# Kernel optimization log

Measured on AMD Instinct MI355X. Metric: run time of the kernel, lower is better.

Reference implementation:

```python
import jax, jax.numpy as jnp
import numpy as np
import math

B, S, HID, H = 1, 2048, 1024, 16
D = HID // H  # head_dim = 64


def setup_inputs() -> dict:
    key = jax.random.key(0)
    ks = jax.random.split(key, 12)
    s = 0.02
    x = jax.random.normal(ks[0], (B, S, HID), jnp.float32)
    Wq = jax.random.normal(ks[1], (HID, HID), jnp.float32) * s
    bq = jnp.zeros((HID,), jnp.float32)
    Wk = jax.random.normal(ks[2], (HID, HID), jnp.float32) * s
    bk = jnp.zeros((HID,), jnp.float32)
    Wv = jax.random.normal(ks[3], (HID, HID), jnp.float32) * s
    bv = jnp.zeros((HID,), jnp.float32)
    Wo = jax.random.normal(ks[4], (HID, HID), jnp.float32) * s
    bo = jnp.zeros((HID,), jnp.float32)
    # nn.Parameter(torch.ones(3,3)) at init; small noise so the bias is non-degenerate
    cmw = jnp.ones((3, 3), jnp.float32) + 0.1 * jax.random.normal(ks[5], (3, 3), jnp.float32)
    # full causal [B,S,S] mask so the mask.shape[1]==seq_len branch is taken
    mask = jnp.tril(jnp.ones((B, S, S), jnp.int32))
    modality_info = jax.random.randint(ks[6], (B, S), 0, 3, dtype=jnp.int64)
    return dict(x=x, Wq=Wq, bq=bq, Wk=Wk, bk=bk, Wv=Wv, bv=bv, Wo=Wo, bo=bo,
                cmw=cmw, mask=mask, modality_info=modality_info)


def reference(x, Wq, bq, Wk, bk, Wv, bv, Wo, bo, cmw, mask, modality_info):
    b, s, _ = x.shape
    # QKV projections (torch Linear: y = x @ W.T + b), split into heads [B,H,S,D]
    q = (x @ Wq.T + bq).reshape(b, s, H, D).transpose(0, 2, 1, 3)
    k = (x @ Wk.T + bk).reshape(b, s, H, D).transpose(0, 2, 1, 3)
    v = (x @ Wv.T + bv).reshape(b, s, H, D).transpose(0, 2, 1, 3)
    scores = jnp.einsum('bhqd,bhkd->bhqk', q, k) / math.sqrt(D)  # [B,H,S,S]
    # cross-modal bias: gather from 3x3 table via pairwise modality indices -> [B,S,S]
    bias = cmw[modality_info[:, :, None], modality_info[:, None, :]]
    scores = scores + bias[:, None, :, :]  # equals original broadcast when B==1
    scores = jnp.where(mask[:, None, :, :] == 0, -1e9, scores)
    attn = jax.nn.softmax(scores, axis=-1)  # dropout is identity in eval
    ctx = jnp.einsum('bhqk,bhkd->bhqd', attn, v)          # [B,H,S,D]
    ctx = ctx.transpose(0, 2, 1, 3).reshape(b, s, HID)    # [B,S,HID]
    return ctx @ Wo.T + bo
```

## Files before the change

### kernel.cpp

```cpp
#include <hip/hip_runtime.h>
#include <hip/hip_bf16.h>
#include <math.h>

#define S_LEN 2048
#define HID   1024
#define NHEAD 16

using bf16x8 = __attribute__((ext_vector_type(8))) short;
using bf16x4 = __attribute__((ext_vector_type(4))) short;
using f32x4  = __attribute__((ext_vector_type(4))) float;

__device__ __forceinline__ float bf2f(short s) {
  union { unsigned u; float f; } c;
  c.u = ((unsigned)(unsigned short)s) << 16;
  return c.f;
}
__device__ __forceinline__ short f2bf(float f) {
  union { float f; unsigned u; } c; c.f = f;
  unsigned u = c.u;
  unsigned r = (u + 0x7fffu + ((u >> 16) & 1u)) >> 16;
  return (short)r;
}
__device__ __forceinline__ void gl_lds16(const void* g, void* l) {
  __builtin_amdgcn_global_load_lds(
      (const __attribute__((address_space(1))) void*)g,
      (__attribute__((address_space(3))) void*)l, 16, 0, 0);
}
__device__ __forceinline__ int detect_bf(const unsigned* xw) {
  int cnt = 0;
#pragma unroll
  for (int i = 0; i < 64; ++i) {
    const unsigned fld = (xw[i] >> 7) & 0xFFu;
    cnt += (fld >= 100u && fld <= 135u) ? 1 : 0;
  }
  return cnt >= 32;
}

__global__ __launch_bounds__(256) void convert10(
    const void* __restrict__ s0, const void* __restrict__ s1, const void* __restrict__ s2,
    const void* __restrict__ s3, const void* __restrict__ s4, const void* __restrict__ s5,
    const void* __restrict__ s6, const void* __restrict__ s7, const void* __restrict__ s8,
    const void* __restrict__ s9,
    short* __restrict__ d0, short* __restrict__ d1, short* __restrict__ d2,
    short* __restrict__ d3, short* __restrict__ d4, short* __restrict__ d5,
    short* __restrict__ d6, short* __restrict__ d7, short* __restrict__ d8,
    short* __restrict__ d9)
{
  const int is_bf = detect_bf((const unsigned*)s0);
  const int a = blockIdx.y;
  const void* src; short* dst; long n;
  if      (a == 0) { src = s0; dst = d0; n = 2L << 20; }
  else if (a == 1) { src = s1; dst = d1; n = 1L << 20; }
  else if (a == 2) { src = s2; dst = d2; n = 1L << 20; }
  else if (a == 3) { src = s3; dst = d3; n = 1L << 20; }
  else if (a == 4) { src = s4; dst = d4; n = 1L << 20; }
  else if (a == 5) { src = s5; dst = d5; n = 1024; }
  else if (a == 6) { src = s6; dst = d6; n = 1024; }
  else if (a == 7) { src = s7; dst = d7; n = 1024; }
  else if (a == 8) { src = s8; dst = d8; n = 1024; }
  else             { src = s9; dst = d9; n = 9; }

  if (n >= 1024) {
    long i = (long)(blockIdx.x * 256 + threadIdx.x) * 8;
    const long stride = (long)gridDim.x * 256 * 8;
    if (is_bf) {
      for (; i < n; i += stride)
        *(bf16x8*)(dst + i) = *(const bf16x8*)((const short*)src + i);
    } else {
      for (; i < n; i += stride) {
        const float* p = (const float*)src + i;
        bf16x8 r;
#pragma unroll
        for (int j = 0; j < 8; ++j) r[j] = f2bf(p[j]);
        *(bf16x8*)(dst + i) = r;
      }
    }
  } else {
    long i = blockIdx.x * 256 + threadIdx.x;
    const long stride = (long)gridDim.x * 256;
    for (; i < n; i += stride)
      dst[i] = is_bf ? ((const short*)src)[i] : f2bf(((const float*)src)[i]);
  }
}

__global__ __launch_bounds__(256) void gemm_bt3(
    const short* __restrict__ A,
    const short* __restrict__ W0, const short* __restrict__ W1, const short* __restrict__ W2,
    const short* __restrict__ b0, const short* __restrict__ b1, const short* __restrict__ b2,
    void* __restrict__ C0, void* __restrict__ C1, void* __restrict__ C2,
    int nbn, int store_f32)
{
  constexpr int K = 1024;
  constexpr int N = 1024;
  __shared__ short As[128 * 32];
  __shared__ short Bs[64 * 32];

  const int t = threadIdx.x;
  const int w = t >> 6, lane = t & 63;
  const int l15 = lane & 15, quad = lane >> 4;
  const int wm = w >> 1, wn = w & 1;

  const int mat = blockIdx.x / nbn;
  const int n0 = (blockIdx.x % nbn) * 64;
  const int m0 = blockIdx.y * 128;

  const short* W  = (mat == 0) ? W0 : (mat == 1 ? W1 : W2);
  const short* bia = (mat == 0) ? b0 : (mat == 1 ? b1 : b2);
  void*       C   = (mat == 0) ? C0 : (mat == 1 ? C1 : C2);

  f32x4 acc[4][2];
  for (int mi = 0; mi < 4; ++mi)
    for (int ni = 0; ni < 2; ++ni)
      for (int r = 0; r < 4; ++r) acc[mi][ni][r] = 0.f;

  const int srow = t >> 2;
  const int sch  = (t & 3) * 8;
  const short* Ap = A + (long)(m0 + srow) * K + sch;
  const short* Wp = W + (long)(n0 + srow) * K + sch;
  short* AsW = &As[w * 512];
  short* BsW = &Bs[w * 512];

  for (int kt = 0; kt < K / 32; ++kt) {
    __syncthreads();
    gl_lds16(Ap + kt * 32, AsW);
    gl_lds16(Ap + kt * 32 + 64L * K, AsW + 2048);
    gl_lds16(Wp + kt * 32, BsW);
    __syncthreads();

    bf16x8 af[4], bfr[2];
    for (int mi = 0; mi < 4; ++mi)
      af[mi] = *(const bf16x8*)&As[(wm * 64 + mi * 16 + l15) * 32 + quad * 8];
    for (int ni = 0; ni < 2; ++ni)
      bfr[ni] = *(const bf16x8*)&Bs[(wn * 32 + ni * 16 + l15) * 32 + quad * 8];
    for (int mi = 0; mi < 4; ++mi)
      for (int ni = 0; ni < 2; ++ni)
        acc[mi][ni] = __builtin_amdgcn_mfma_f32_16x16x32_bf16(af[mi], bfr[ni], acc[mi][ni], 0, 0, 0);
  }

  for (int ni = 0; ni < 2; ++ni) {
    const int col = n0 + wn * 32 + ni * 16 + l15;
    const float bv = bf2f(bia[col]);
    for (int mi = 0; mi < 4; ++mi) {
      const int row = m0 + wm * 64 + mi * 16 + quad * 4;
      for (int r = 0; r < 4; ++r) {
        const float v = acc[mi][ni][r] + bv;
        const long idx = (long)(row + r) * N + col;
        if (store_f32) ((float*)C)[idx] = v;
        else           ((short*)C)[idx] = f2bf(v);
      }
    }
  }
}

__global__ __launch_bounds__(256) void attn_split(
    const short* __restrict__ Q, const short* __restrict__ Kg, const short* __restrict__ Vg,
    const int* __restrict__ mod, const short* __restrict__ cmw,
    short* __restrict__ PO0, short* __restrict__ PO1,
    float* __restrict__ PL)
{
  __shared__ short Ks[2][64 * 80];
  __shared__ short Vt[2][64 * 80];
  __shared__ short Ps[4 * 16 * 80];
  __shared__ float cm[9];
  __shared__ int mods[2048];

  const int t = threadIdx.x;
  const int w = t >> 6, lane = t & 63;
  const int l15 = lane & 15, quad = lane >> 4;
  const int h = blockIdx.y;
  const int pair = blockIdx.x >> 1;
  const int par  = blockIdx.x & 1;

  int oddbits = 0;
#pragma unroll
  for (int i = 0; i < 64; ++i) oddbits |= mod[2 * i + 1];
  const int m64 = (oddbits == 0) ? 1 : 0;

  if (t < 9) cm[t] = bf2f(cmw[t]);
  for (int i = t; i < 2048; i += 256) mods[i] = mod[i << m64];
  __syncthreads();

  short* POp = (par == 0) ? PO0 : PO1;
  short* Pw = &Ps[w * 16 * 80];
  const int krow = t >> 3, kch = (t & 7) * 8;
  const int vkp = t & 63, vdc = (t >> 6) * 8;

  for (int si = 0; si < 2; ++si) {
    const int strip = (si == 0) ? pair : 31 - pair;
    const int q0 = strip * 64;
    const int nkt = strip + 1;

    const short* qb = Q + (long)(q0 + w * 16 + l15) * HID + h * 64 + quad * 8;
    const bf16x8 aq0 = *(const bf16x8*)qb;
    const bf16x8 aq1 = *(const bf16x8*)(qb + 32);

    int mrow[4];
    for (int r = 0; r < 4; ++r) mrow[r] = mods[q0 + w * 16 + quad * 4 + r];

    float lsum[4];
    f32x4 acc_o[4];
    for (int r = 0; r < 4; ++r) lsum[r] = 0.f;
    for (int ni = 0; ni < 4; ++ni)
      for (int r = 0; r < 4; ++r) acc_o[ni][r] = 0.f;

    bf16x8 rkA[2], rvA[2], rkB[2], rvB[2];
    auto ldtile = [&](int kt_, bf16x8* rk, bf16x8* rv) {
      const long kb = (long)(kt_ * 64) * HID + h * 64;
      rk[0] = *(const bf16x8*)(Kg + kb + (long)krow * HID + kch);
      rk[1] = *(const bf16x8*)(Kg + kb + (long)(krow + 32) * HID + kch);
      rv[0] = *(const bf16x8*)(Vg + kb + (long)vkp * HID + vdc);
      rv[1] = *(const bf16x8*)(Vg + kb + (long)vkp * HID + 32 + vdc);
    };
    auto sttile = [&](int buf, bf16x8* rk, bf16x8* rv) {
      *(bf16x8*)&Ks[buf][krow * 80 + kch] = rk[0];
      *(bf16x8*)&Ks[buf][(krow + 32) * 80 + kch] = rk[1];
#pragma unroll
      for (int j = 0; j < 8; ++j) Vt[buf][(vdc + j) * 80 + vkp] = rv[0][j];
#pragma unroll
      for (int j = 0; j < 8; ++j) Vt[buf][(vdc + 32 + j) * 80 + vkp] = rv[1][j];
    };
    auto tile_compute = [&](int kt_, int buf) {
      f32x4 sc[4];
      for (int nt = 0; nt < 4; ++nt) {
        const bf16x8 kb0 = *(const bf16x8*)&Ks[buf][(nt * 16 + l15) * 80 + quad * 8];
        const bf16x8 kb1 = *(const bf16x8*)&Ks[buf][(nt * 16 + l15) * 80 + 32 + quad * 8];
        f32x4 z;
        for (int r = 0; r < 4; ++r) z[r] = 0.f;
        z = __builtin_amdgcn_mfma_f32_16x16x32_bf16(aq0, kb0, z, 0, 0, 0);
        z = __builtin_amdgcn_mfma_f32_16x16x32_bf16(aq1, kb1, z, 0, 0, 0);
        sc[nt] = z;
      }
      float sv[4][4];
      for (int nt = 0; nt < 4; ++nt) {
        const int mcol = mods[kt_ * 64 + nt * 16 + l15];
        for (int r = 0; r < 4; ++r)
          sv[nt][r] = sc[nt][r] * 0.125f + cm[mrow[r] * 3 + mcol];
      }
      if (kt_ == nkt - 1) {
        for (int nt = 0; nt < 4; ++nt) {
          const int col = kt_ * 64 + nt * 16 + l15;
          for (int r = 0; r < 4; ++r) {
            const int row = q0 + w * 16 + quad * 4 + r;
            sv[nt][r] = (col <= row) ? sv[nt][r] : -1e30f;
          }
        }
      }
      short pb[4][4];
      for (int nt = 0; nt < 4; ++nt)
        for (int r = 0; r < 4; ++r) {
          const float p = __expf(fminf(sv[nt][r], 60.f));
          lsum[r] += p;
          pb[nt][r] = f2bf(p);
        }
      for (int nt = 0; nt < 4; ++nt)
        for (int r = 0; r < 4; ++r)
          Pw[(quad * 4 + r) * 80 + nt * 16 + l15] = pb[nt][r];
      asm volatile("s_waitcnt lgkmcnt(0)" ::: "memory");
      for (int kk = 0; kk < 2; ++kk) {
        const bf16x8 ap = *(const bf16x8*)&Pw[l15 * 80 + kk * 32 + quad * 8];
        for (int ni = 0; ni < 4; ++ni) {
          const bf16x8 bv = *(const bf16x8*)&Vt[buf][(ni * 16 + l15) * 80 + kk * 32 + quad * 8];
          acc_o[ni] = __builtin_amdgcn_mfma_f32_16x16x32_bf16(ap, bv, acc_o[ni], 0, 0, 0);
        }
      }
    };

    if (par < nkt)     ldtile(par, rkA, rvA);
    if (par + 2 < nkt) ldtile(par + 2, rkB, rvB);

    for (int kt = par; kt < nkt; kt += 4) {
      const bool has2 = (kt + 2 < nkt);
      __syncthreads();
      sttile(0, rkA, rvA);
      if (has2) sttile(1, rkB, rvB);
      __syncthreads();
      if (kt + 4 < nkt) ldtile(kt + 4, rkA, rvA);
      if (kt + 6 < nkt) ldtile(kt + 6, rkB, rvB);
      tile_compute(kt, 0);
      if (has2) tile_compute(kt + 2, 1);
    }

    for (int off = 1; off < 16; off <<= 1)
      for (int r = 0; r < 4; ++r) lsum[r] += __shfl_xor(lsum[r], off);

    for (int ni = 0; ni < 4; ++ni) {
      const int col = h * 64 + ni * 16 + l15;
      for (int r = 0; r < 4; ++r) {
        const int row = q0 + w * 16 + quad * 4 + r;
        POp[(long)row * HID + col] = f2bf(acc_o[ni][r]);
      }
    }
    if (l15 == 0) {
      for (int r = 0; r < 4; ++r) {
        const int row = q0 + w * 16 + quad * 4 + r;
        PL[par * 32768 + row * 16 + h] = lsum[r];
      }
    }
  }
}

__global__ __launch_bounds__(256) void attn_merge(
    const short* __restrict__ PO0, const short* __restrict__ PO1,
    const float* __restrict__ PL, short* __restrict__ CTX)
{
  const int row = blockIdx.x;
  const int t = threadIdx.x;
  const int h = t >> 4;
  const int d0 = (t & 15) * 4;
  const float l0 = PL[row * 16 + h], l1 = PL[32768 + row * 16 + h];
  const float inv = 1.f / (l0 + l1);
  const long b = (long)row * HID + h * 64 + d0;
  const bf16x4 o0 = *(const bf16x4*)&PO0[b];
  const bf16x4 o1 = *(const bf16x4*)&PO1[b];
  bf16x4 out;
#pragma unroll
  for (int j = 0; j < 4; ++j)
    out[j] = f2bf((bf2f(o0[j]) + bf2f(o1[j])) * inv);
  *(bf16x4*)&CTX[b] = out;
}

extern "C" void kernel_launch(void* const* d_in, const int* in_sizes, int n_in,
                              void* d_out, int out_size, void* d_ws, size_t ws_size,
                              hipStream_t stream) {
  constexpr long M1 = 1024L * 1024L;
  short* ws = (short*)d_ws;
  short* xb  = ws;
  short* Wqb = xb + 2 * M1;
  short* Wkb = Wqb + M1;
  short* Wvb = Wkb + M1;
  short* Wob = Wvb + M1;
  short* Qw  = Wob + M1;
  short* Kw  = Qw + 2 * M1;
  short* Vw  = Kw + 2 * M1;
  short* CTX = Vw + 2 * M1;
  short* bqb = CTX + 2 * M1;
  short* bkb = bqb + 1024;
  short* bvb = bkb + 1024;
  short* bob = bvb + 1024;
  short* cmb = bob + 1024;
  short* PO0 = CTX;
  short* PO1 = xb;
  float* PL  = (float*)Wvb;
  const int* modality = (const int*)d_in[11];

  convert10<<<dim3(256, 10), 256, 0, stream>>>(
      d_in[0], d_in[1], d_in[3], d_in[5], d_in[7],
      d_in[2], d_in[4], d_in[6], d_in[8], d_in[9],
      xb, Wqb, Wkb, Wvb, Wob, bqb, bkb, bvb, bob, cmb);

  gemm_bt3<<<dim3(48, 16), 256, 0, stream>>>(
      xb, Wqb, Wkb, Wvb, bqb, bkb, bvb,
      Qw, Kw, Vw, 16, 0);
  attn_split<<<dim3(32, NHEAD), 256, 0, stream>>>(
      Qw, Kw, Vw, modality, cmb, PO0, PO1, PL);
  attn_merge<<<dim3(S_LEN), 256, 0, stream>>>(PO0, PO1, PL, CTX);
  gemm_bt3<<<dim3(16, 16), 256, 0, stream>>>(
      CTX, Wob, Wob, Wob, bob, bob, bob,
      d_out, d_out, d_out, 16, 1);
}
```

Before: 183.2 us.

## Fuse attention split-merge into output projection GEMM and register-prefetch GEMM tiles

```diff
diff --git a/kernel.cpp b/kernel.cpp
--- a/kernel.cpp
+++ b/kernel.cpp
@@ -20,11 +20,6 @@
   unsigned u = c.u;
   unsigned r = (u + 0x7fffu + ((u >> 16) & 1u)) >> 16;
   return (short)r;
-}
-__device__ __forceinline__ void gl_lds16(const void* g, void* l) {
-  __builtin_amdgcn_global_load_lds(
-      (const __attribute__((address_space(1))) void*)g,
-      (__attribute__((address_space(3))) void*)l, 16, 0, 0);
 }
 __device__ __forceinline__ int detect_bf(const unsigned* xw) {
   int cnt = 0;
@@ -87,8 +82,8 @@
     const short* __restrict__ A,
     const short* __restrict__ W0, const short* __restrict__ W1, const short* __restrict__ W2,
     const short* __restrict__ b0, const short* __restrict__ b1, const short* __restrict__ b2,
-    void* __restrict__ C0, void* __restrict__ C1, void* __restrict__ C2,
-    int nbn, int store_f32)
+    short* __restrict__ C0, short* __restrict__ C1, short* __restrict__ C2,
+    int nbn)
 {
   constexpr int K = 1024;
   constexpr int N = 1024;
@@ -104,9 +99,9 @@
   const int n0 = (blockIdx.x % nbn) * 64;
   const int m0 = blockIdx.y * 128;
 
-  const short* W  = (mat == 0) ? W0 : (mat == 1 ? W1 : W2);
+  const short* W   = (mat == 0) ? W0 : (mat == 1 ? W1 : W2);
   const short* bia = (mat == 0) ? b0 : (mat == 1 ? b1 : b2);
-  void*       C   = (mat == 0) ? C0 : (mat == 1 ? C1 : C2);
+  short*       C   = (mat == 0) ? C0 : (mat == 1 ? C1 : C2);
 
   f32x4 acc[4][2];
   for (int mi = 0; mi < 4; ++mi)
@@ -117,16 +112,22 @@
   const int sch  = (t & 3) * 8;
   const short* Ap = A + (long)(m0 + srow) * K + sch;
   const short* Wp = W + (long)(n0 + srow) * K + sch;
-  short* AsW = &As[w * 512];
-  short* BsW = &Bs[w * 512];
+
+  bf16x8 ra0 = *(const bf16x8*)(Ap);
+  bf16x8 ra1 = *(const bf16x8*)(Ap + 64L * K);
+  bf16x8 rb0 = *(const bf16x8*)(Wp);
 
   for (int kt = 0; kt < K / 32; ++kt) {
     __syncthreads();
-    gl_lds16(Ap + kt * 32, AsW);
-    gl_lds16(Ap + kt * 32 + 64L * K, AsW + 2048);
-    gl_lds16(Wp + kt * 32, BsW);
+    *(bf16x8*)&As[(srow)      * 32 + sch] = ra0;
+    *(bf16x8*)&As[(srow + 64) * 32 + sch] = ra1;
+    *(bf16x8*)&Bs[(srow)      * 32 + sch] = rb0;
     __syncthreads();
-
+    if (kt + 1 < K / 32) {
+      ra0 = *(const bf16x8*)(Ap + (kt + 1) * 32);
+      ra1 = *(const bf16x8*)(Ap + (kt + 1) * 32 + 64L * K);
+      rb0 = *(const bf16x8*)(Wp + (kt + 1) * 32);
+    }
     bf16x8 af[4], bfr[2];
     for (int mi = 0; mi < 4; ++mi)
       af[mi] = *(const bf16x8*)&As[(wm * 64 + mi * 16 + l15) * 32 + quad * 8];
@@ -142,12 +143,8 @@
     const float bv = bf2f(bia[col]);
     for (int mi = 0; mi < 4; ++mi) {
       const int row = m0 + wm * 64 + mi * 16 + quad * 4;
-      for (int r = 0; r < 4; ++r) {
-        const float v = acc[mi][ni][r] + bv;
-        const long idx = (long)(row + r) * N + col;
-        if (store_f32) ((float*)C)[idx] = v;
-        else           ((short*)C)[idx] = f2bf(v);
-      }
+      for (int r = 0; r < 4; ++r)
+        C[(long)(row + r) * N + col] = f2bf(acc[mi][ni][r] + bv);
     }
   }
 }
@@ -299,24 +296,89 @@
   }
 }
 
-__global__ __launch_bounds__(256) void attn_merge(
+__global__ __launch_bounds__(256) void gemm_omerge(
     const short* __restrict__ PO0, const short* __restrict__ PO1,
-    const float* __restrict__ PL, short* __restrict__ CTX)
+    const float* __restrict__ PL,
+    const short* __restrict__ W, const short* __restrict__ bia,
+    float* __restrict__ C)
 {
-  const int row = blockIdx.x;
+  constexpr int K = 1024;
+  constexpr int N = 1024;
+  __shared__ short As[128 * 32];
+  __shared__ short Bs[64 * 32];
+
   const int t = threadIdx.x;
-  const int h = t >> 4;
-  const int d0 = (t & 15) * 4;
-  const float l0 = PL[row * 16 + h], l1 = PL[32768 + row * 16 + h];
-  const float inv = 1.f / (l0 + l1);
-  const long b = (long)row * HID + h * 64 + d0;
-  const bf16x4 o0 = *(const bf16x4*)&PO0[b];
-  const bf16x4 o1 = *(const bf16x4*)&PO1[b];
-  bf16x4 out;
-#pragma unroll
-  for (int j = 0; j < 4; ++j)
-    out[j] = f2bf((bf2f(o0[j]) + bf2f(o1[j])) * inv);
-  *(bf16x4*)&CTX[b] = out;
+  const int w = t >> 6, lane = t & 63;
+  const int l15 = lane & 15, quad = lane >> 4;
+  const int wm = w >> 1, wn = w & 1;
+
+  const int n0 = blockIdx.x * 64;
+  const int m0 = blockIdx.y * 128;
+
+  f32x4 acc[4][2];
+  for (int mi = 0; mi < 4; ++mi)
+    for (int ni = 0; ni < 2; ++ni)
+      for (int r = 0; r < 4; ++r) acc[mi][ni][r] = 0.f;
+
+  const int srow = t >> 2;
+  const int sch  = (t & 3) * 8;
+  const int r0 = m0 + srow, r1 = m0 + srow + 64;
+  const long a0 = (long)r0 * K + sch;
+  const long a1 = (long)r1 * K + sch;
+  const short* Wp = W + (long)(n0 + srow) * K + sch;
+
+  bf16x8 p00 = *(const bf16x8*)(PO0 + a0);
+  bf16x8 p01 = *(const bf16x8*)(PO1 + a0);
+  bf16x8 p10 = *(const bf16x8*)(PO0 + a1);
+  bf16x8 p11 = *(const bf16x8*)(PO1 + a1);
+  bf16x8 rb0 = *(const bf16x8*)(Wp);
+  float il0 = 1.f / (PL[r0 * 16] + PL[32768 + r0 * 16]);
+  float il1 = 1.f / (PL[r1 * 16] + PL[32768 + r1 * 16]);
+
+  for (int kt = 0; kt < K / 32; ++kt) {
+    __syncthreads();
+    {
+      bf16x8 m0v, m1v;
+#pragma unroll
+      for (int j = 0; j < 8; ++j) {
+        m0v[j] = f2bf((bf2f(p00[j]) + bf2f(p01[j])) * il0);
+        m1v[j] = f2bf((bf2f(p10[j]) + bf2f(p11[j])) * il1);
+      }
+      *(bf16x8*)&As[(srow)      * 32 + sch] = m0v;
+      *(bf16x8*)&As[(srow + 64) * 32 + sch] = m1v;
+      *(bf16x8*)&Bs[(srow)      * 32 + sch] = rb0;
+    }
+    __syncthreads();
+    if (kt + 1 < K / 32) {
+      const long kb = (long)(kt + 1) * 32;
+      p00 = *(const bf16x8*)(PO0 + a0 + kb);
+      p01 = *(const bf16x8*)(PO1 + a0 + kb);
+      p10 = *(const bf16x8*)(PO0 + a1 + kb);
+      p11 = *(const bf16x8*)(PO1 + a1 + kb);
+      rb0 = *(const bf16x8*)(Wp + kb);
+      const int hh = (kt + 1) >> 1;
+      il0 = 1.f / (PL[r0 * 16 + hh] + PL[32768 + r0 * 16 + hh]);
+      il1 = 1.f / (PL[r1 * 16 + hh] + PL[32768 + r1 * 16 + hh]);
+    }
+    bf16x8 af[4], bfr[2];
+    for (int mi = 0; mi < 4; ++mi)
+      af[mi] = *(const bf16x8*)&As[(wm * 64 + mi * 16 + l15) * 32 + quad * 8];
+    for (int ni = 0; ni < 2; ++ni)
+      bfr[ni] = *(const bf16x8*)&Bs[(wn * 32 + ni * 16 + l15) * 32 + quad * 8];
+    for (int mi = 0; mi < 4; ++mi)
+      for (int ni = 0; ni < 2; ++ni)
+        acc[mi][ni] = __builtin_amdgcn_mfma_f32_16x16x32_bf16(af[mi], bfr[ni], acc[mi][ni], 0, 0, 0);
+  }
+
+  for (int ni = 0; ni < 2; ++ni) {
+    const int col = n0 + wn * 32 + ni * 16 + l15;
+    const float bv = bf2f(bia[col]);
+    for (int mi = 0; mi < 4; ++mi) {
+      const int row = m0 + wm * 64 + mi * 16 + quad * 4;
+      for (int r = 0; r < 4; ++r)
+        C[(long)(row + r) * N + col] = acc[mi][ni][r] + bv;
+    }
+  }
 }
 
 extern "C" void kernel_launch(void* const* d_in, const int* in_sizes, int n_in,
@@ -332,13 +394,12 @@
   short* Qw  = Wob + M1;
   short* Kw  = Qw + 2 * M1;
   short* Vw  = Kw + 2 * M1;
-  short* CTX = Vw + 2 * M1;
-  short* bqb = CTX + 2 * M1;
+  short* PO0 = Vw + 2 * M1;
+  short* bqb = PO0 + 2 * M1;
   short* bkb = bqb + 1024;
   short* bvb = bkb + 1024;
   short* bob = bvb + 1024;
   short* cmb = bob + 1024;
-  short* PO0 = CTX;
   short* PO1 = xb;
   float* PL  = (float*)Wvb;
   const int* modality = (const int*)d_in[11];
@@ -349,12 +410,9 @@
       xb, Wqb, Wkb, Wvb, Wob, bqb, bkb, bvb, bob, cmb);
 
   gemm_bt3<<<dim3(48, 16), 256, 0, stream>>>(
-      xb, Wqb, Wkb, Wvb, bqb, bkb, bvb,
-      Qw, Kw, Vw, 16, 0);
+      xb, Wqb, Wkb, Wvb, bqb, bkb, bvb, Qw, Kw, Vw, 16);
   attn_split<<<dim3(32, NHEAD), 256, 0, stream>>>(
       Qw, Kw, Vw, modality, cmb, PO0, PO1, PL);
-  attn_merge<<<dim3(S_LEN), 256, 0, stream>>>(PO0, PO1, PL, CTX);
-  gemm_bt3<<<dim3(16, 16), 256, 0, stream>>>(
-      CTX, Wob, Wob, Wob, bob, bob, bob,
-      d_out, d_out, d_out, 16, 1);
-}
+  gemm_omerge<<<dim3(16, 16), 256, 0, stream>>>(
+      PO0, PO1, PL, Wob, bob, (float*)d_out);
+}
```

Result: slower. 189.7 us (+3.5%).
